# Performance work log

Measured on AMD Instinct MI355X. Metric: run time of the kernel, lower is better.

Reference implementation:

```python
import jax, jax.numpy as jnp
import numpy as np

K = 3          # deform conv kernel size (hard-coded in module)
DILATE = 1     # padding == dilation for the deform conv


def conv2d(x, w, b, pad, dil):
    y = jax.lax.conv_general_dilated(
        x, w, window_strides=(1, 1),
        padding=[(pad, pad), (pad, pad)],
        rhs_dilation=(dil, dil),
        dimension_numbers=("NCHW", "OIHW", "NCHW"))
    return y + b[None, :, None, None]


def setup_inputs() -> dict:
    key = jax.random.key(0)
    k0, k1, k2 = jax.random.split(key, 3)
    B, C, H, W, O = 4, 64, 128, 128, 64
    x = jax.random.normal(k0, (B, C, H, W), jnp.float32)
    fan_off = C * 9
    w_off = jax.random.normal(k1, (2 * K * K, C, 3, 3), jnp.float32) / np.float32(np.sqrt(fan_off))
    b_off = jnp.zeros((2 * K * K,), jnp.float32)
    w_def = jax.random.normal(k2, (O, C, K, K), jnp.float32) / np.float32(np.sqrt(C * K * K))
    b_def = jnp.zeros((O,), jnp.float32)
    return {"x": x, "w_off": w_off, "b_off": b_off, "w_def": w_def, "b_def": b_def}


def deform_conv2d(x, off, w_def, b_def, dilate):
    # off: [B, 2*K*K, H, W] with (dy, dx) interleaved per kernel position
    B, C, H, W = x.shape
    off = off.reshape(B, K * K, 2, H, W)

    ky, kx = jnp.meshgrid(jnp.arange(K), jnp.arange(K), indexing="ij")
    ky = ((ky.reshape(-1) - (K // 2)) * dilate)  # [K*K], since padding == dilation
    kx = ((kx.reshape(-1) - (K // 2)) * dilate)
    hh, ww = jnp.meshgrid(jnp.arange(H), jnp.arange(W), indexing="ij")  # [H, W]

    # sampling positions [B, K*K, H, W]
    py = off[:, :, 0] + (hh[None, None] + ky[None, :, None, None]).astype(x.dtype)
    px = off[:, :, 1] + (ww[None, None] + kx[None, :, None, None]).astype(x.dtype)

    y0f = jnp.floor(py); x0f = jnp.floor(px)
    ly = py - y0f; lx = px - x0f
    y0 = y0f.astype(jnp.int32); x0 = x0f.astype(jnp.int32)

    xf = x.reshape(B, C, H * W)

    def gather(yi, xi):
        valid = ((yi >= 0) & (yi < H) & (xi >= 0) & (xi < W)).astype(x.dtype)
        idx = jnp.clip(yi, 0, H - 1) * W + jnp.clip(xi, 0, W - 1)  # [B, K*K, H, W]
        g = jax.vmap(lambda xb, ib: xb[:, ib.reshape(-1)])(xf, idx)  # [B, C, K*K*H*W]
        return g.reshape(B, C, K * K, H, W) * valid[:, None]

    w00 = ((1 - ly) * (1 - lx))[:, None]
    w01 = ((1 - ly) * lx)[:, None]
    w10 = (ly * (1 - lx))[:, None]
    w11 = (ly * lx)[:, None]

    samp = (gather(y0, x0) * w00 + gather(y0, x0 + 1) * w01 +
            gather(y0 + 1, x0) * w10 + gather(y0 + 1, x0 + 1) * w11)  # [B,C,K*K,H,W]

    out = jnp.einsum("bckhw,ock->bohw", samp, w_def.reshape(w_def.shape[0], C, K * K))
    return out + b_def[None, :, None, None]


def reference(x, w_off, b_off, w_def, b_def):
    off = conv2d(x, w_off, b_off, pad=1, dil=1)     # offset conv, 3x3, pad=1
    off = jnp.clip(off, -1.0, 1.0)                  # Hardtanh
    return deform_conv2d(x, off, w_def, b_def, DILATE)
```

## Files before the change

kernel.cpp:

```cpp
#include <hip/hip_runtime.h>

typedef _Float16 f16;
typedef __attribute__((ext_vector_type(8))) _Float16 f16x8;
typedef __attribute__((ext_vector_type(4))) _Float16 f16x4;
typedef __attribute__((ext_vector_type(4))) float f32x4;

#define HWB 16384


__device__ __forceinline__ void prep_elem(int i,
                                          const float* __restrict__ w_off,
                                          const float* __restrict__ w_def,
                                          f16* __restrict__ wdef_ap,
                                          f16* __restrict__ woff_ap) {
    if (i < 36864) {
        int j = i & 7, l = (i >> 3) & 63, m = (i >> 9) & 3, t = i >> 11;
        int kk = t >> 1, ch = t & 1;
        int o = m * 16 + (l & 15);
        int c = ch * 32 + (l >> 4) * 8 + j;
        wdef_ap[i] = (f16)w_def[o * 576 + c * 9 + kk];
    } else if (i < 55296) {
        int i2 = i - 36864;
        int j = i2 & 7, l = (i2 >> 3) & 63, m = (i2 >> 9) & 1, t = i2 >> 10;
        int kk = t >> 1, ch = t & 1;
        int o = m * 16 + (l & 15);
        int c = ch * 32 + (l >> 4) * 8 + j;
        woff_ap[i2] = (f16)((o < 18) ? w_off[o * 576 + c * 9 + kk] : 0.f);
    }
}

__global__ void k_prep(const float* __restrict__ w_off,
                       const float* __restrict__ w_def,
                       f16* __restrict__ wdef_ap,
                       f16* __restrict__ woff_ap) {
    prep_elem(blockIdx.x * 256 + threadIdx.x, w_off, w_def, wdef_ap, woff_ap);
}

__global__ void k_xprep(const float* __restrict__ x, f16* __restrict__ xt,
                        const float* __restrict__ w_off,
                        const float* __restrict__ w_def,
                        f16* __restrict__ wdef_ap,
                        f16* __restrict__ woff_ap) {
    int p = blockIdx.x * 256 + threadIdx.x;
    prep_elem(p, w_off, w_def, wdef_ap, woff_ap);
    int b = p >> 14, hw = p & 16383;
    const float* xb = x + (size_t)b * 64 * HWB + hw;
    f16x8 r[8];
    #pragma unroll
    for (int c = 0; c < 64; ++c) r[c >> 3][c & 7] = (f16)xb[(size_t)c * HWB];
    f16* ob = xt + (size_t)p * 64;
    #pragma unroll
    for (int q = 0; q < 8; ++q) *(f16x8*)(ob + q * 8) = r[q];
}

__global__ void k_xpose(const float* __restrict__ x, f16* __restrict__ xt) {
    int p = blockIdx.x * 256 + threadIdx.x;
    const float* xb = x + p;
    f16x8 r[8];
    #pragma unroll
    for (int c = 0; c < 64; ++c) r[c >> 3][c & 7] = (f16)xb[(size_t)c * HWB];
    f16* ob = xt + (size_t)p * 64;
    #pragma unroll
    for (int q = 0; q < 8; ++q) *(f16x8*)(ob + q * 8) = r[q];
}

__launch_bounds__(256, 4)
__global__ void k_fused(const f16* __restrict__ xt,
                        const f16* __restrict__ woff_ap,
                        const float* __restrict__ b_off,
                        const f16* __restrict__ wdef_ap,
                        const float* __restrict__ b_def,
                        float* __restrict__ out, int bstart) {
    __shared__ __align__(16) char band[6 * 40 * 128];
    __shared__ float offsm[18 * 33];
    __shared__ float red0[8 * 128];
    float* red1 = (float*)band;

    int nwg = gridDim.x;
    int bid = blockIdx.x;
    int sb = (bid & 7) * (nwg >> 3) + (bid >> 3);
    int bl = sb >> 9, h = (sb >> 2) & 127, quarter = sb & 3;
    int b = bstart + bl;
    int s = quarter * 32;
    int tid = threadIdx.x;
    int lane = tid & 63, wv = tid >> 6;
    int pxg = wv & 1, chh = wv >> 1;
    int l15 = lane & 15, g = lane >> 4;
    int pxl = pxg * 16 + l15;
    int pxb = s + pxl;
    int rlane = pxg * 64 + lane;

    const f16* xb = xt + (size_t)bl * HWB * 64;
    unsigned co = (unsigned)((chh * 4 + g) * 16);

    {
        int cell_lo = lane >> 3, cc = lane & 7;
        for (int gid = wv; gid < 30; gid += 4) {
            int r = gid / 5, seg = gid - (gid / 5) * 5;
            int cell0 = seg * 8;
            int cell = cell0 + cell_lo;
            int y = min(max(h - 2 + r, 0), 127);
            int xg = min(max(s - 2 + cell, 0), 127);
            int gg = cc ^ (cell & 7);
            const f16* gsrc = xb + (size_t)((y * 128 + xg) * 64 + gg * 8);
            char* ldst = band + (r * 40 + cell0) * 128;
            if (cell < 37)
                __builtin_amdgcn_global_load_lds(
                    (const __attribute__((address_space(1))) unsigned int*)gsrc,
                    (__attribute__((address_space(3))) unsigned int*)ldst,
                    16, 0, 0);
        }
    }
    __syncthreads();

    f32x4 oacc[2];
    {
        f32x4 z = {0.f, 0.f, 0.f, 0.f};
        oacc[0] = z; oacc[1] = z;
    }
    f16x8 zb = {};
    #pragma unroll
    for (int kk = 0; kk < 9; ++kk) {
        int ky = kk / 3 - 1, kx = kk - (kk / 3) * 3 - 1;
        int yy = h + ky, xx = pxb + kx;
        bool valid = ((unsigned)yy < 128u) && ((unsigned)xx < 128u);
        int ry = min(max(yy, 0), 127) - (h - 2);
        int cx = min(max(xx, 0), 127) - (s - 2);
        f16x8 B = *(const f16x8*)(band + (ry * 40 + cx) * 128 +
                                  (co ^ (((unsigned)cx & 7u) << 4)));
        B = valid ? B : zb;
        int t = kk * 2 + chh;
        #pragma unroll
        for (int m = 0; m < 2; ++m) {
            f16x8 A = *(const f16x8*)(woff_ap + ((size_t)(t * 2 + m) * 64 + lane) * 8);
            oacc[m] = __builtin_amdgcn_mfma_f32_16x16x32_f16(A, B, oacc[m], 0, 0, 0);
        }
    }
    if (chh == 1) {
        #pragma unroll
        for (int m = 0; m < 2; ++m)
            #pragma unroll
            for (int r = 0; r < 4; ++r) red0[(m * 4 + r) * 128 + rlane] = oacc[m][r];
    }
    __syncthreads();
    if (chh == 0) {
        #pragma unroll
        for (int m = 0; m < 2; ++m)
            #pragma unroll
            for (int r = 0; r < 4; ++r) {
                int o = m * 16 + g * 4 + r;
                if (o < 18) {
                    float v = oacc[m][r] + red0[(m * 4 + r) * 128 + rlane] + b_off[o];
                    offsm[o * 33 + pxl] = fminf(fmaxf(v, -1.f), 1.f);
                }
            }
    }
    __syncthreads();

    f16x4 wq[9];
    unsigned a0[9], a1[9], a2[9], a3[9];
    #pragma unroll
    for (int kk = 0; kk < 9; ++kk) {
        float dy = offsm[(2 * kk) * 33 + pxl];
        float dx = offsm[(2 * kk + 1) * 33 + pxl];
        int ky = kk / 3 - 1, kx = kk - (kk / 3) * 3 - 1;
        float py = (float)(h + ky) + dy;
        float pxf = (float)(pxb + kx) + dx;
        float y0f = floorf(py), x0f = floorf(pxf);
        float ly = py - y0f, lx = pxf - x0f;
        int y0 = (int)y0f, x0 = (int)x0f;
        float vy0 = ((unsigned)y0 < 128u) ? 1.f : 0.f;
        float vy1 = ((unsigned)(y0 + 1) < 128u) ? 1.f : 0.f;
        float vx0 = ((unsigned)x0 < 128u) ? 1.f : 0.f;
        float vx1 = ((unsigned)(x0 + 1) < 128u) ? 1.f : 0.f;
        wq[kk][0] = (f16)((1.f - ly) * (1.f - lx) * vy0 * vx0);
        wq[kk][1] = (f16)((1.f - ly) * lx * vy0 * vx1);
        wq[kk][2] = (f16)(ly * (1.f - lx) * vy1 * vx0);
        wq[kk][3] = (f16)(ly * lx * vy1 * vx1);
        int yc0 = min(max(y0, 0), 127), yc1 = min(max(y0 + 1, 0), 127);
        int xc0 = min(max(x0, 0), 127), xc1 = min(max(x0 + 1, 0), 127);
        int ry0 = yc0 - (h - 2), ry1 = yc1 - (h - 2);
        int cx0 = xc0 - (s - 2), cx1 = xc1 - (s - 2);
        unsigned s0 = co ^ (((unsigned)cx0 & 7u) << 4);
        unsigned s1 = co ^ (((unsigned)cx1 & 7u) << 4);
        a0[kk] = (unsigned)((ry0 * 40 + cx0) * 128) + s0;
        a1[kk] = (unsigned)((ry0 * 40 + cx1) * 128) + s1;
        a2[kk] = (unsigned)((ry1 * 40 + cx0) * 128) + s0;
        a3[kk] = (unsigned)((ry1 * 40 + cx1) * 128) + s1;
    }

    f32x4 acc[4];
    {
        f32x4 z = {0.f, 0.f, 0.f, 0.f};
        acc[0] = z; acc[1] = z; acc[2] = z; acc[3] = z;
    }
    #pragma unroll
    for (int kk = 0; kk < 9; ++kk) {
        f16x8 c00 = *(const f16x8*)(band + a0[kk]);
        f16x8 c01 = *(const f16x8*)(band + a1[kk]);
        f16x8 c10 = *(const f16x8*)(band + a2[kk]);
        f16x8 c11 = *(const f16x8*)(band + a3[kk]);
        f16x8 B = c00 * wq[kk][0] + c01 * wq[kk][1] +
                  c10 * wq[kk][2] + c11 * wq[kk][3];
        int t = kk * 2 + chh;
        #pragma unroll
        for (int m = 0; m < 4; ++m) {
            f16x8 A = *(const f16x8*)(wdef_ap + ((size_t)(t * 4 + m) * 64 + lane) * 8);
            acc[m] = __builtin_amdgcn_mfma_f32_16x16x32_f16(A, B, acc[m], 0, 0, 0);
        }
    }

    __syncthreads();
    if (chh == 1) {
        #pragma unroll
        for (int m = 0; m < 4; ++m)
            #pragma unroll
            for (int r = 0; r < 4; ++r) red1[(m * 4 + r) * 128 + rlane] = acc[m][r];
    }
    __syncthreads();
    if (chh == 0) {
        #pragma unroll
        for (int m = 0; m < 4; ++m)
            #pragma unroll
            for (int r = 0; r < 4; ++r) {
                int o = m * 16 + g * 4 + r;
                float v = acc[m][r] + red1[(m * 4 + r) * 128 + rlane] + b_def[o];
                out[(size_t)(b * 64 + o) * HWB + h * 128 + pxb] = v;
            }
    }
}

extern "C" void kernel_launch(void* const* d_in, const int* in_sizes, int n_in,
                              void* d_out, int out_size, void* d_ws, size_t ws_size,
                              hipStream_t stream) {
    const float* x     = (const float*)d_in[0];
    const float* w_off = (const float*)d_in[1];
    const float* b_off = (const float*)d_in[2];
    const float* w_def = (const float*)d_in[3];
    const float* b_def = (const float*)d_in[4];
    float* out = (float*)d_out;

    char* wsb = (char*)d_ws;
    f16* wdef_ap = (f16*)wsb;
    f16* woff_ap = (f16*)(wsb + 73728);
    f16* xt      = (f16*)(wsb + 110592);

    if (ws_size >= (size_t)110592 + 8388608) {
        k_xprep<<<256, 256, 0, stream>>>(x, xt, w_off, w_def, wdef_ap, woff_ap);
        k_fused<<<2048, 256, 0, stream>>>(xt, woff_ap, b_off, wdef_ap, b_def, out, 0);
    } else {
        k_prep<<<216, 256, 0, stream>>>(w_off, w_def, wdef_ap, woff_ap);
        for (int b = 0; b < 4; ++b) {
            k_xpose<<<64, 256, 0, stream>>>(x + (size_t)b * 64 * HWB, xt);
            k_fused<<<512, 256, 0, stream>>>(xt, woff_ap, b_off, wdef_ap, b_def, out, b);
        }
    }
}
```

Before: 37.41 us.

## Switch MFMA tiling to 32x32x16 with four-way channel split across waves

Replaces the 16x16x32 MFMA tiling (2 pixel groups x 2 channel halves per block) with 32x32x16 MFMA, where each wave covers all 32 pixels and a quarter of the channels. Both weight layouts are repacked to match. The split-K partials from three waves are reduced through shared memory by wave 0. This halves the MFMA instruction count and A-operand loads, but makes the reduction serial over three partial buffers and concentrates the epilogue (bias, clamp, output stores) in one wave.

Result: faster. 36.22 us (-3.2%).

```diff
diff --git a/kernel.cpp b/kernel.cpp
--- a/kernel.cpp
+++ b/kernel.cpp
@@ -3,7 +3,7 @@
 typedef _Float16 f16;
 typedef __attribute__((ext_vector_type(8))) _Float16 f16x8;
 typedef __attribute__((ext_vector_type(4))) _Float16 f16x4;
-typedef __attribute__((ext_vector_type(4))) float f32x4;
+typedef __attribute__((ext_vector_type(16))) float f32x16;
 
 #define HWB 16384
 
@@ -14,17 +14,17 @@
                                           f16* __restrict__ wdef_ap,
                                           f16* __restrict__ woff_ap) {
     if (i < 36864) {
-        int j = i & 7, l = (i >> 3) & 63, m = (i >> 9) & 3, t = i >> 11;
-        int kk = t >> 1, ch = t & 1;
-        int o = m * 16 + (l & 15);
-        int c = ch * 32 + (l >> 4) * 8 + j;
+        int j = i & 7, l = (i >> 3) & 63, m = (i >> 9) & 1;
+        int chq = (i >> 10) & 3, kk = i >> 12;
+        int o = m * 32 + (l & 31);
+        int c = chq * 16 + (l >> 5) * 8 + j;
         wdef_ap[i] = (f16)w_def[o * 576 + c * 9 + kk];
     } else if (i < 55296) {
         int i2 = i - 36864;
-        int j = i2 & 7, l = (i2 >> 3) & 63, m = (i2 >> 9) & 1, t = i2 >> 10;
-        int kk = t >> 1, ch = t & 1;
-        int o = m * 16 + (l & 15);
-        int c = ch * 32 + (l >> 4) * 8 + j;
+        int j = i2 & 7, l = (i2 >> 3) & 63;
+        int chq = (i2 >> 9) & 3, kk = i2 >> 11;
+        int o = l & 31;
+        int c = chq * 16 + (l >> 5) * 8 + j;
         woff_ap[i2] = (f16)((o < 18) ? w_off[o * 576 + c * 9 + kk] : 0.f);
     }
 }
@@ -73,7 +73,7 @@
                         float* __restrict__ out, int bstart) {
     __shared__ __align__(16) char band[6 * 40 * 128];
     __shared__ float offsm[18 * 33];
-    __shared__ float red0[8 * 128];
+    __shared__ float red0[3 * 594];
     float* red1 = (float*)band;
 
     int nwg = gridDim.x;
@@ -83,19 +83,16 @@
     int b = bstart + bl;
     int s = quarter * 32;
     int tid = threadIdx.x;
-    int lane = tid & 63, wv = tid >> 6;
-    int pxg = wv & 1, chh = wv >> 1;
-    int l15 = lane & 15, g = lane >> 4;
-    int pxl = pxg * 16 + l15;
-    int pxb = s + pxl;
-    int rlane = pxg * 64 + lane;
+    int lane = tid & 63, chq = tid >> 6;
+    int px = lane & 31, half = lane >> 5;
+    int pxb = s + px;
 
     const f16* xb = xt + (size_t)bl * HWB * 64;
-    unsigned co = (unsigned)((chh * 4 + g) * 16);
+    unsigned co = (unsigned)((chq * 2 + half) * 16);
 
     {
         int cell_lo = lane >> 3, cc = lane & 7;
-        for (int gid = wv; gid < 30; gid += 4) {
+        for (int gid = chq; gid < 30; gid += 4) {
             int r = gid / 5, seg = gid - (gid / 5) * 5;
             int cell0 = seg * 8;
             int cell = cell0 + cell_lo;
@@ -113,11 +110,7 @@
     }
     __syncthreads();
 
-    f32x4 oacc[2];
-    {
-        f32x4 z = {0.f, 0.f, 0.f, 0.f};
-        oacc[0] = z; oacc[1] = z;
-    }
+    f32x16 oacc = {};
     f16x8 zb = {};
     #pragma unroll
     for (int kk = 0; kk < 9; ++kk) {
@@ -129,31 +122,28 @@
         f16x8 B = *(const f16x8*)(band + (ry * 40 + cx) * 128 +
                                   (co ^ (((unsigned)cx & 7u) << 4)));
         B = valid ? B : zb;
-        int t = kk * 2 + chh;
-        #pragma unroll
-        for (int m = 0; m < 2; ++m) {
-            f16x8 A = *(const f16x8*)(woff_ap + ((size_t)(t * 2 + m) * 64 + lane) * 8);
-            oacc[m] = __builtin_amdgcn_mfma_f32_16x16x32_f16(A, B, oacc[m], 0, 0, 0);
-        }
-    }
-    if (chh == 1) {
-        #pragma unroll
-        for (int m = 0; m < 2; ++m)
-            #pragma unroll
-            for (int r = 0; r < 4; ++r) red0[(m * 4 + r) * 128 + rlane] = oacc[m][r];
-    }
-    __syncthreads();
-    if (chh == 0) {
-        #pragma unroll
-        for (int m = 0; m < 2; ++m)
-            #pragma unroll
-            for (int r = 0; r < 4; ++r) {
-                int o = m * 16 + g * 4 + r;
-                if (o < 18) {
-                    float v = oacc[m][r] + red0[(m * 4 + r) * 128 + rlane] + b_off[o];
-                    offsm[o * 33 + pxl] = fminf(fmaxf(v, -1.f), 1.f);
-                }
+        f16x8 A = *(const f16x8*)(woff_ap + ((size_t)(kk * 4 + chq) * 64 + lane) * 8);
+        oacc = __builtin_amdgcn_mfma_f32_32x32x16_f16(A, B, oacc, 0, 0, 0);
+    }
+    if (chq != 0) {
+        #pragma unroll
+        for (int reg = 0; reg < 16; ++reg) {
+            int row = (reg & 3) + 8 * (reg >> 2) + 4 * half;
+            if (row < 18) red0[(chq - 1) * 594 + row * 33 + px] = oacc[reg];
+        }
+    }
+    __syncthreads();
+    if (chq == 0) {
+        #pragma unroll
+        for (int reg = 0; reg < 16; ++reg) {
+            int row = (reg & 3) + 8 * (reg >> 2) + 4 * half;
+            if (row < 18) {
+                float v = oacc[reg] + red0[row * 33 + px] +
+                          red0[594 + row * 33 + px] + red0[1188 + row * 33 + px] +
+                          b_off[row];
+                offsm[row * 33 + px] = fminf(fmaxf(v, -1.f), 1.f);
             }
+        }
     }
     __syncthreads();
 
@@ -161,8 +151,8 @@
     unsigned a0[9], a1[9], a2[9], a3[9];
     #pragma unroll
     for (int kk = 0; kk < 9; ++kk) {
-        float dy = offsm[(2 * kk) * 33 + pxl];
-        float dx = offsm[(2 * kk + 1) * 33 + pxl];
+        float dy = offsm[(2 * kk) * 33 + px];
+        float dx = offsm[(2 * kk + 1) * 33 + px];
         int ky = kk / 3 - 1, kx = kk - (kk / 3) * 3 - 1;
         float py = (float)(h + ky) + dy;
         float pxf = (float)(pxb + kx) + dx;
@@ -189,11 +179,7 @@
         a3[kk] = (unsigned)((ry1 * 40 + cx1) * 128) + s1;
     }
 
-    f32x4 acc[4];
-    {
-        f32x4 z = {0.f, 0.f, 0.f, 0.f};
-        acc[0] = z; acc[1] = z; acc[2] = z; acc[3] = z;
-    }
+    f32x16 acc0 = {}, acc1 = {};
     #pragma unroll
     for (int kk = 0; kk < 9; ++kk) {
         f16x8 c00 = *(const f16x8*)(band + a0[kk]);
@@ -202,29 +188,34 @@
         f16x8 c11 = *(const f16x8*)(band + a3[kk]);
         f16x8 B = c00 * wq[kk][0] + c01 * wq[kk][1] +
                   c10 * wq[kk][2] + c11 * wq[kk][3];
-        int t = kk * 2 + chh;
-        #pragma unroll
-        for (int m = 0; m < 4; ++m) {
-            f16x8 A = *(const f16x8*)(wdef_ap + ((size_t)(t * 4 + m) * 64 + lane) * 8);
-            acc[m] = __builtin_amdgcn_mfma_f32_16x16x32_f16(A, B, acc[m], 0, 0, 0);
-        }
-    }
-
-    __syncthreads();
-    if (chh == 1) {
-        #pragma unroll
-        for (int m = 0; m < 4; ++m)
+        size_t tb = (size_t)((kk * 4 + chq) * 2) * 64 * 8;
+        f16x8 A0 = *(const f16x8*)(wdef_ap + tb + (size_t)lane * 8);
+        f16x8 A1 = *(const f16x8*)(wdef_ap + tb + (size_t)(64 + lane) * 8);
+        acc0 = __builtin_amdgcn_mfma_f32_32x32x16_f16(A0, B, acc0, 0, 0, 0);
+        acc1 = __builtin_amdgcn_mfma_f32_32x32x16_f16(A1, B, acc1, 0, 0, 0);
+    }
+
+    __syncthreads();
+    if (chq != 0) {
+        #pragma unroll
+        for (int m = 0; m < 2; ++m)
             #pragma unroll
-            for (int r = 0; r < 4; ++r) red1[(m * 4 + r) * 128 + rlane] = acc[m][r];
-    }
-    __syncthreads();
-    if (chh == 0) {
-        #pragma unroll
-        for (int m = 0; m < 4; ++m)
+            for (int reg = 0; reg < 16; ++reg) {
+                int o = m * 32 + (reg & 3) + 8 * (reg >> 2) + 4 * half;
+                float v = m ? acc1[reg] : acc0[reg];
+                red1[(chq - 1) * 2112 + o * 33 + px] = v;
+            }
+    }
+    __syncthreads();
+    if (chq == 0) {
+        #pragma unroll
+        for (int m = 0; m < 2; ++m)
             #pragma unroll
-            for (int r = 0; r < 4; ++r) {
-                int o = m * 16 + g * 4 + r;
-                float v = acc[m][r] + red1[(m * 4 + r) * 128 + rlane] + b_def[o];
+            for (int reg = 0; reg < 16; ++reg) {
+                int o = m * 32 + (reg & 3) + 8 * (reg >> 2) + 4 * half;
+                float v = (m ? acc1[reg] : acc0[reg]) +
+                          red1[o * 33 + px] + red1[2112 + o * 33 + px] +
+                          red1[4224 + o * 33 + px] + b_def[o];
                 out[(size_t)(b * 64 + o) * HWB + h * 128 + pxb] = v;
             }
     }
```
